# Kernel optimization log

Hardware: AMD Instinct MI355X
Metric: run time of the kernel (lower is better)

## Reference

```python
import jax, jax.numpy as jnp
import numpy as np

L = 4      # layer_num
H = 4      # n_head
C = 64     # emb_dim
E = 8      # ceil(512/65) Q/K channels per head
CV = 16    # emb_dim // n_head, V channels per head
FQ = 65    # n_freqs
EPS = 1e-5


def setup_inputs() -> dict:
    key = jax.random.key(0)
    ks = jax.random.split(key, 12)
    B, Tp, Tn = 4, 400, 400
    w = lambda k, shape, s=0.05: jax.random.normal(k, shape, jnp.float32) * s
    return {
        "pos_cond": jax.random.normal(ks[0], (B, C, Tp, FQ), jnp.float32),
        "neg_cond": jax.random.normal(ks[1], (B, C, Tn, FQ), jnp.float32),
        "seg_table": w(ks[2], (2, C * FQ), 0.02),
        # per-layer, per-head Q/K/V conv1x1 + PReLU + LayerNorm4DCF params
        "Qw": w(ks[3], (L, H, E, C)),  "Qb": jnp.zeros((L, H, E), jnp.float32),
        "Qa": jnp.full((L, H), 0.25, jnp.float32),
        "Qg": jnp.ones((L, H, E, FQ), jnp.float32), "Qbe": jnp.zeros((L, H, E, FQ), jnp.float32),
        "Kw": w(ks[4], (L, H, E, C)),  "Kb": jnp.zeros((L, H, E), jnp.float32),
        "Ka": jnp.full((L, H), 0.25, jnp.float32),
        "Kg": jnp.ones((L, H, E, FQ), jnp.float32), "Kbe": jnp.zeros((L, H, E, FQ), jnp.float32),
        "Vw": w(ks[5], (L, H, CV, C)), "Vb": jnp.zeros((L, H, CV), jnp.float32),
        "Va": jnp.full((L, H), 0.25, jnp.float32),
        "Vg": jnp.ones((L, H, CV, FQ), jnp.float32), "Vbe": jnp.zeros((L, H, CV, FQ), jnp.float32),
        # per-layer concat projection conv1x1 + PReLU + LayerNorm4DCF
        "Pw": w(ks[6], (L, C, C)), "Pb": jnp.zeros((L, C), jnp.float32),
        "Pa": jnp.full((L,), 0.25, jnp.float32),
        "Pg": jnp.ones((L, C, FQ), jnp.float32), "Pbe": jnp.zeros((L, C, FQ), jnp.float32),
    }


def _head_proj(x, W, b, a, g, be):
    # x: [B,C,T,F]; W: [H,O,C] -> y: [H,B,O,T,F]; conv1x1 + PReLU(scalar) + LN over (channel,freq)
    y = jnp.einsum('bctf,hoc->hbotf', x, W) + b[:, None, :, None, None]
    y = jnp.where(y >= 0, y, a[:, None, None, None, None] * y)
    mu = jnp.mean(y, axis=(2, 4), keepdims=True)
    var = jnp.var(y, axis=(2, 4), keepdims=True)
    return (y - mu) / jnp.sqrt(var + EPS) * g[:, None, :, None, :] + be[:, None, :, None, :]


def _attn_layer(x, Qw, Qb, Qa, Qg, Qbe, Kw, Kb, Ka, Kg, Kbe, Vw, Vb, Va, Vg, Vbe, Pw, Pb, Pa, Pg, Pbe):
    B, _, T, F = x.shape
    Q = _head_proj(x, Qw, Qb, Qa, Qg, Qbe)   # [H,B,E,T,F]
    K = _head_proj(x, Kw, Kb, Ka, Kg, Kbe)   # [H,B,E,T,F]
    V = _head_proj(x, Vw, Vb, Va, Vg, Vbe)   # [H,B,CV,T,F]
    Qf = jnp.transpose(Q, (0, 1, 3, 2, 4)).reshape(H, B, T, E * F)
    Kf = jnp.transpose(K, (0, 1, 3, 2, 4)).reshape(H, B, T, E * F)
    Vf = jnp.transpose(V, (0, 1, 3, 2, 4)).reshape(H, B, T, CV * F)
    d = Qf.shape[-1]
    attn = jax.nn.softmax(jnp.einsum('hbtd,hbsd->hbts', Qf, Kf) / jnp.sqrt(jnp.float32(d)), axis=-1)
    Of = jnp.einsum('hbts,hbsd->hbtd', attn, Vf)              # [H,B,T,CV*F]
    O = Of.reshape(H, B, T, CV, F)
    O = jnp.transpose(O, (1, 0, 3, 2, 4)).reshape(B, H * CV, T, F)  # concat heads on channel
    # concat projection: conv1x1 + PReLU + LN4DCF
    y = jnp.einsum('bctf,oc->botf', O, Pw) + Pb[None, :, None, None]
    y = jnp.where(y >= 0, y, Pa * y)
    mu = jnp.mean(y, axis=(1, 3), keepdims=True)
    var = jnp.var(y, axis=(1, 3), keepdims=True)
    return (y - mu) / jnp.sqrt(var + EPS) * Pg[None, :, None, :] + Pbe[None, :, None, :]


def reference(pos_cond, neg_cond, seg_table, Qw, Qb, Qa, Qg, Qbe, Kw, Kb, Ka, Kg, Kbe,
              Vw, Vb, Va, Vg, Vbe, Pw, Pb, Pa, Pg, Pbe):
    B, _, Tp, _ = pos_cond.shape
    Tn = neg_cond.shape[2]
    T = Tp + Tn
    x = jnp.concatenate([pos_cond, neg_cond], axis=2)          # [B,C,T,F]
    seg_idx = jnp.concatenate([jnp.zeros((Tp,), jnp.int32), jnp.ones((Tn,), jnp.int32)])
    seg = seg_table[seg_idx].reshape(T, C, FQ)                 # [T,C,F]
    x = x + jnp.transpose(seg, (1, 0, 2))[None]                # [1,C,T,F] broadcast over B
    fusion_shortcut = (0,)
    for li in range(L):
        y = _attn_layer(x, Qw[li], Qb[li], Qa[li], Qg[li], Qbe[li],
                        Kw[li], Kb[li], Ka[li], Kg[li], Kbe[li],
                        Vw[li], Vb[li], Va[li], Vg[li], Vbe[li],
                        Pw[li], Pb[li], Pa[li], Pg[li], Pbe[li])
        x = x + y if li in fusion_shortcut else y
    return x
```

## Files before the change

### kernel.cpp

```cpp
#include <hip/hip_runtime.h>

#define BB 4
#define CC 64
#define TT 800
#define FF 65
#define EE 8
#define CVV 16
#define HH 4

typedef __attribute__((ext_vector_type(8))) short short8;
typedef __attribute__((ext_vector_type(4))) float f32x4;

#define OT_SLAB (800 * 68 * 16)

__device__ __forceinline__ float bf2f(unsigned short u) {
  unsigned v = ((unsigned)u) << 16;
  return __builtin_bit_cast(float, v);
}
__device__ __forceinline__ unsigned short f2bf(float f) {
  unsigned u = __builtin_bit_cast(unsigned, f);
  unsigned r = (u + 0x7fffu + ((u >> 16) & 1u)) >> 16;
  return (unsigned short)r;
}

__device__ __forceinline__ void gll16(const void* g, void* l) {
  __builtin_amdgcn_global_load_lds(
      (const __attribute__((address_space(1))) void*)g,
      (__attribute__((address_space(3))) void*)l, 16, 0, 0);
}

__global__ __launch_bounds__(256) void buildx_kernel(
    const float* __restrict__ pos, const float* __restrict__ neg,
    const float* __restrict__ seg, float* __restrict__ X)
{
  size_t i = (size_t)blockIdx.x * 256 + threadIdx.x;
  const size_t total = (size_t)BB * CC * TT * FF;
  if (i >= total) return;
  int f = (int)(i % FF);
  size_t r = i / FF;
  int t = (int)(r % TT);
  size_t r2 = r / TT;
  int c = (int)(r2 % CC);
  int b = (int)(r2 / CC);
  float v; int si;
  if (t < 400) { v = pos[(((size_t)b * CC + c) * 400 + t) * FF + f]; si = 0; }
  else         { v = neg[(((size_t)b * CC + c) * 400 + (t - 400)) * FF + f]; si = 1; }
  X[i] = v + seg[(size_t)si * CC * FF + c * FF + f];
}

__global__ __launch_bounds__(256) void xt0_kernel(
    const float* __restrict__ X, unsigned short* __restrict__ Xt)
{
  __shared__ unsigned short tile[64][66];
  int b = blockIdx.y;
  int p0 = blockIdx.x * 64;
  int tid = threadIdx.x;
#pragma unroll
  for (int it = 0; it < 16; ++it) {
    int idx = it * 256 + tid;
    int c = idx >> 6, pp = idx & 63;
    int ps = p0 + pp;
    float v = (ps < 52000) ? X[((size_t)b * 64 + c) * 52000 + ps] : 0.f;
    tile[pp][c] = f2bf(v);
  }
  __syncthreads();
#pragma unroll
  for (int it = 0; it < 16; ++it) {
    int idx = it * 256 + tid;
    int pp = idx >> 6, c = idx & 63;
    int ps = p0 + pp;
    Xt[((size_t)b * 52032 + ps) * 64 + c] = tile[pp][c];
  }
}

__global__ __launch_bounds__(512) void qkv_gemm_kernel(
    const unsigned short* __restrict__ Xt,
    const float* __restrict__ Qw, const float* __restrict__ Qb, const float* __restrict__ Qa,
    const float* __restrict__ Qg, const float* __restrict__ Qbe,
    const float* __restrict__ Kw, const float* __restrict__ Kbi, const float* __restrict__ Ka,
    const float* __restrict__ Kg, const float* __restrict__ Kbe,
    const float* __restrict__ Vw, const float* __restrict__ Vb, const float* __restrict__ Va,
    const float* __restrict__ Vg, const float* __restrict__ Vbe,
    unsigned short* __restrict__ Qo, unsigned short* __restrict__ Ko,
    unsigned short* __restrict__ Vo, int li)
{
  __shared__ __align__(16) unsigned short lds[26624];
  unsigned short* lA = lds;

  int wg = (blockIdx.x & 7) * 100 + (blockIdx.x >> 3);
  int b = wg & 3, tb = wg >> 2;
  int tid = threadIdx.x;
  int lane = tid & 63, wid = tid >> 6;
  int tp = wid >> 2;
  int ws2 = wid & 3;
  int t0 = tb * 4 + tp * 2;
  unsigned short* lB = lds + 8192 + tp * 9216;

  for (int i = tid; i < 896; i += 512) {
    int u = i / 28, c = i - u * 28;
    int h = u >> 3, arr = (u >> 2) & 1, tt = u & 3;
    unsigned short* bp = arr ? Ko : Qo;
    unsigned* dst = (unsigned*)(bp + ((size_t)(h * 4 + b) * 896 + tb * 4 + tt) * 576) + 260 + c;
    *dst = 0u;
  }

  const float* Wq = Qw + (size_t)li * 2048;
  const float* Wk = Kw + (size_t)li * 2048;
  const float* Wv = Vw + (size_t)li * 4096;
#pragma unroll
  for (int q = 0; q < 2; ++q) {
    int chunk = q * 512 + tid;
    int row = chunk >> 3, c8 = chunk & 7;
    const float* src = (row < 32) ? (Wq + row * 64)
                     : (row < 64) ? (Wk + (row - 32) * 64)
                                  : (Wv + (row - 64) * 64);
    float4 f0 = *(const float4*)(src + c8 * 8);
    float4 f1 = *(const float4*)(src + c8 * 8 + 4);
    uint4 u;
    u.x = (unsigned)f2bf(f0.x) | ((unsigned)f2bf(f0.y) << 16);
    u.y = (unsigned)f2bf(f0.z) | ((unsigned)f2bf(f0.w) << 16);
    u.z = (unsigned)f2bf(f1.x) | ((unsigned)f2bf(f1.y) << 16);
    u.w = (unsigned)f2bf(f1.z) | ((unsigned)f2bf(f1.w) << 16);
    *(uint4*)&lA[row * 64 + ((c8 * 8) ^ ((row & 7) << 3))] = u;
  }
  const unsigned short* xb = Xt + ((size_t)b * 52032 + tb * 260) * 64;
#pragma unroll
  for (int q = 0; q < 5; ++q) {
    int chunk = q * 512 + tid;
    if (chunk < 2304) {
      int pair = (chunk >= 1152) ? 1 : 0;
      int ch = chunk - pair * 1152;
      int row = ch >> 3, c8 = ch & 7;
      uint4 u = *(const uint4*)&xb[(size_t)(pair * 130 + row) * 64 + c8 * 8];
      unsigned short* lbp = lds + 8192 + pair * 9216;
      *(uint4*)&lbp[row * 64 + ((c8 * 8) ^ ((row & 7) << 3))] = u;
    }
  }
  __syncthreads();

  f32x4 acc[2][9];
#pragma unroll
  for (int i = 0; i < 2; ++i)
#pragma unroll
    for (int j = 0; j < 9; ++j) acc[i][j] = {0.f, 0.f, 0.f, 0.f};
  const int fr = lane & 15, fk = lane >> 4;
  const int swz = (lane & 7) << 3;
#pragma unroll
  for (int kk = 0; kk < 2; ++kk) {
    int ko = (kk * 32 + fk * 8) ^ swz;
    short8 a0 = *(const short8*)&lA[(ws2 * 32 + fr) * 64 + ko];
    short8 a1 = *(const short8*)&lA[(ws2 * 32 + 16 + fr) * 64 + ko];
#pragma unroll
    for (int nf = 0; nf < 9; ++nf) {
      short8 bfr = *(const short8*)&lB[(nf * 16 + fr) * 64 + ko];
      acc[0][nf] = __builtin_amdgcn_mfma_f32_16x16x32_bf16(a0, bfr, acc[0][nf], 0, 0, 0);
      acc[1][nf] = __builtin_amdgcn_mfma_f32_16x16x32_bf16(a1, bfr, acc[1][nf], 0, 0, 0);
    }
  }
  __syncthreads();

  for (int it = 0; it < 17; ++it) {
    int i = it * 512 + tid;
    if (i < 8320) {
      int row = i / 65;
      float g, be;
      if (i < 2080)      { g = Qg[li * 2080 + i];          be = Qbe[li * 2080 + i]; }
      else if (i < 4160) { g = Kg[li * 2080 + (i - 2080)]; be = Kbe[li * 2080 + (i - 2080)]; }
      else               { g = Vg[li * 4160 + (i - 4160)]; be = Vbe[li * 4160 + (i - 4160)]; }
      unsigned pk = (unsigned)f2bf(g) | ((unsigned)f2bf(be) << 16);
      *(unsigned*)&lds[(i + row) * 2] = pk;
    }
  }

  int r4 = (lane >> 4) * 4;
  float mu0_[2], rs0_[2], mu1_[2], rs1_[2];
#pragma unroll
  for (int mf2 = 0; mf2 < 2; ++mf2) {
    int rbase = ws2 * 32 + mf2 * 16 + r4;
    float bias[4], alpha;
    if (rbase < 32) {
      alpha = Qa[li * 4 + (rbase >> 3)];
#pragma unroll
      for (int j = 0; j < 4; ++j) bias[j] = Qb[li * 32 + rbase + j];
    } else if (rbase < 64) {
      alpha = Ka[li * 4 + ((rbase - 32) >> 3)];
#pragma unroll
      for (int j = 0; j < 4; ++j) bias[j] = Kbi[li * 32 + rbase - 32 + j];
    } else {
      alpha = Va[li * 4 + ((rbase - 64) >> 4)];
#pragma unroll
      for (int j = 0; j < 4; ++j) bias[j] = Vb[li * 64 + rbase - 64 + j];
    }
    float s0 = 0.f, ss0 = 0.f, s1 = 0.f, ss1 = 0.f;
#pragma unroll
    for (int nf = 0; nf < 9; ++nf) {
      int col = nf * 16 + fr;
#pragma unroll
      for (int j = 0; j < 4; ++j) {
        float v = acc[mf2][nf][j] + bias[j];
        v = v >= 0.f ? v : alpha * v;
        acc[mf2][nf][j] = v;
        if (col < 65) { s0 += v; ss0 += v * v; }
        else if (col < 130) { s1 += v; ss1 += v * v; }
      }
    }
    if (ws2 < 2) {
#pragma unroll
      for (int off = 1; off < 32; off <<= 1) {
        s0 += __shfl_xor(s0, off); ss0 += __shfl_xor(ss0, off);
        s1 += __shfl_xor(s1, off); ss1 += __shfl_xor(ss1, off);
      }
    } else {
#pragma unroll
      for (int off = 1; off < 64; off <<= 1) {
        s0 += __shfl_xor(s0, off); ss0 += __shfl_xor(ss0, off);
        s1 += __shfl_xor(s1, off); ss1 += __shfl_xor(ss1, off);
      }
    }
    float invn = (ws2 < 2) ? (1.f / 520.f) : (1.f / 1040.f);
    float m0v = s0 * invn, m1v = s1 * invn;
    mu0_[mf2] = m0v; rs0_[mf2] = rsqrtf(ss0 * invn - m0v * m0v + 1e-5f);
    mu1_[mf2] = m1v; rs1_[mf2] = rsqrtf(ss1 * invn - m1v * m1v + 1e-5f);
  }
  __syncthreads();

#pragma unroll
  for (int mf2 = 0; mf2 < 2; ++mf2) {
#pragma unroll
    for (int j = 0; j < 4; ++j) {
      int row = ws2 * 32 + mf2 * 16 + r4 + j;
      unsigned short* dst; int LD;
      if (row < 32) {
        dst = Qo + ((size_t)((row >> 3) * 4 + b) * 896 + t0) * 576 + (row & 7) * 65; LD = 576;
      } else if (row < 64) {
        int rk = row - 32;
        dst = Ko + ((size_t)((rk >> 3) * 4 + b) * 896 + t0) * 576 + (rk & 7) * 65; LD = 576;
      } else {
        int rv = row - 64;
        dst = Vo + ((size_t)((rv >> 4) * 4 + b) * 800 + t0) * 1040 + (rv & 15) * 65; LD = 1040;
      }
      int grow = row * 132;
#pragma unroll
      for (int nf = 0; nf < 9; ++nf) {
        int col = nf * 16 + fr;
        if (col >= 130) continue;
        int half = (col >= 65) ? 1 : 0;
        int f = col - half * 65;
        unsigned pk = *(const unsigned*)&lds[grow + f * 2];
        float g = bf2f((unsigned short)(pk & 0xffff));
        float be = bf2f((unsigned short)(pk >> 16));
        float mu = half ? mu1_[mf2] : mu0_[mf2];
        float rs = half ? rs1_[mf2] : rs0_[mf2];
        dst[(size_t)half * LD + f] = f2bf((acc[mf2][nf][j] - mu) * rs * g + be);
      }
    }
  }
}

__global__ __launch_bounds__(256) void vtrans_kernel(
    const unsigned short* __restrict__ V, unsigned short* __restrict__ Vt)
{
  __shared__ unsigned short tile[64][66];
  int z = blockIdx.z;
  const unsigned short* Vp = V + (size_t)z * 800 * 1040;
  unsigned short* Vtp = Vt + (size_t)z * 1152 * 832;
  int t0 = blockIdx.x * 64, n0 = blockIdx.y * 64;
  int tid = threadIdx.x;
#pragma unroll
  for (int it = 0; it < 16; ++it) {
    int idx = it * 256 + tid;
    int r = idx >> 6, c = idx & 63;
    int t = t0 + r, n = n0 + c;
    tile[r][c] = (t < 800 && n < 1040) ? Vp[(size_t)t * 1040 + n] : (unsigned short)0;
  }
  __syncthreads();
#pragma unroll
  for (int it = 0; it < 16; ++it) {
    int idx = it * 256 + tid;
    int r = idx >> 6, c = idx & 63;
    int n = n0 + r;
    if (n < 1040) {
      int cv = n / 65, f5 = n - cv * 65;
      Vtp[(size_t)(f5 * 16 + cv) * 832 + t0 + c] = tile[c][r];
    }
  }
}

template <int LDA, int LDB, int KSTEPS>
__device__ __forceinline__ void gemm128(
    const unsigned short* __restrict__ Ag, const unsigned short* __restrict__ Bg,
    int m0, int n0, unsigned short* lA, unsigned short* lB, f32x4 acc[4][4])
{
  const int tid = threadIdx.x;
  const int lane = tid & 63;
  const int wid = tid >> 6;
  const int wm = wid >> 1, wn = wid & 1;

  const int fr = lane & 15, fk = lane >> 4;
  const int swz = (lane & 7) << 3;
  const int srow = lane >> 3;
  const int gc8 = (lane & 7) ^ srow;
  int aoff[4][2], boff[4][2];
#pragma unroll
  for (int mf = 0; mf < 4; ++mf)
#pragma unroll
    for (int kk = 0; kk < 2; ++kk) {
      aoff[mf][kk] = (wm * 64 + mf * 16 + fr) * 64 + ((kk * 32 + fk * 8) ^ swz);
      boff[mf][kk] = (wn * 64 + mf * 16 + fr) * 64 + ((kk * 32 + fk * 8) ^ swz);
    }

  const unsigned short* gA = Ag + (size_t)m0 * LDA;
  const unsigned short* gB = Bg + (size_t)n0 * LDB;

  for (int ks = 0; ks < KSTEPS; ++ks) {
    int k0 = ks * 64;
    __syncthreads();
#pragma unroll
    for (int i = 0; i < 4; ++i) {
      int r0 = wid * 32 + i * 8;
      gll16(&gA[(size_t)(r0 + srow) * LDA + k0 + gc8 * 8], &lA[r0 * 64]);
      gll16(&gB[(size_t)(r0 + srow) * LDB + k0 + gc8 * 8], &lB[r0 * 64]);
    }
    __syncthreads();
#pragma unroll
    for (int kk = 0; kk < 2; ++kk) {
      short8 a[4], b[4];
#pragma unroll
      for (int i = 0; i < 4; ++i) {
        a[i] = *(const short8*)&lA[aoff[i][kk]];
        b[i] = *(const short8*)&lB[boff[i][kk]];
      }
#pragma unroll
      for (int i = 0; i < 4; ++i)
#pragma unroll
        for (int j = 0; j < 4; ++j)
          acc[i][j] = __builtin_amdgcn_mfma_f32_16x16x32_bf16(a[i], b[j], acc[i][j], 0, 0, 0);
    }
  }
}

__global__ __launch_bounds__(256) void qk_mfma_kernel(
    const unsigned short* __restrict__ Q, const unsigned short* __restrict__ K,
    unsigned short* __restrict__ SP)
{
  __shared__ __align__(16) unsigned short lA[128 * 64];
  __shared__ __align__(16) unsigned short lB[128 * 64];
  int wg = (blockIdx.x & 7) * 98 + (blockIdx.x >> 3);
  int z = wg / 49, r = wg % 49;
  int nt = r / 7, mt = r % 7;
  const unsigned short* Ag = Q + (size_t)z * 896 * 576;
  const unsigned short* Bg = K + (size_t)z * 896 * 576;
  int m0 = mt * 128, n0 = nt * 128;
  f32x4 acc[4][4];
#pragma unroll
  for (int i = 0; i < 4; ++i)
#pragma unroll
    for (int j = 0; j < 4; ++j) acc[i][j] = {0.f, 0.f, 0.f, 0.f};
  gemm128<576, 576, 9>(Ag, Bg, m0, n0, lA, lB, acc);
  const int lane = threadIdx.x & 63, wid = threadIdx.x >> 6;
  const int wm = wid >> 1, wn = wid & 1;
  unsigned short* Sp = SP + (size_t)z * 896 * 832;
  const float scale = 0.04385290096535146f;
#pragma unroll
  for (int mf = 0; mf < 4; ++mf)
#pragma unroll
    for (int nf = 0; nf < 4; ++nf) {
      int n = n0 + wn * 64 + nf * 16 + (lane & 15);
      if (n >= 800) continue;
#pragma unroll
      for (int j = 0; j < 4; ++j) {
        int m = m0 + wm * 64 + mf * 16 + (lane >> 4) * 4 + j;
        if (m < 800) Sp[(size_t)m * 832 + n] = f2bf(acc[mf][nf][j] * scale);
      }
    }
}

__global__ __launch_bounds__(256) void softmax_bf16_kernel(unsigned short* __restrict__ SP)
{
  int wid = threadIdx.x >> 6, lane = threadIdx.x & 63;
  int row = blockIdx.x * 4 + wid;
  int z = row / 800, r = row - z * 800;
  unsigned short* p = SP + (size_t)z * 896 * 832 + (size_t)r * 832;
  float v[13];
  float mx = -1e30f;
#pragma unroll
  for (int i = 0; i < 13; ++i) {
    int col = i * 64 + lane;
    float x = (col < 800) ? bf2f(p[col]) : -1e30f;
    v[i] = x;
    mx = fmaxf(mx, x);
  }
#pragma unroll
  for (int off = 32; off; off >>= 1) mx = fmaxf(mx, __shfl_xor(mx, off));
  float s = 0.f;
#pragma unroll
  for (int i = 0; i < 13; ++i) { v[i] = __expf(v[i] - mx); s += v[i]; }
#pragma unroll
  for (int off = 32; off; off >>= 1) s += __shfl_xor(s, off);
  float inv = 1.0f / s;
#pragma unroll
  for (int i = 0; i < 13; ++i) {
    int col = i * 64 + lane;
    if (col < 832) p[col] = f2bf(v[i] * inv);
  }
}

__global__ __launch_bounds__(256) void pv_mfma_kernel(
    const unsigned short* __restrict__ SP, const unsigned short* __restrict__ Vt,
    unsigned short* __restrict__ Ot)
{
  __shared__ __align__(16) unsigned short lA[128 * 64];
  __shared__ __align__(16) unsigned short lB[128 * 64];
  int wg = (blockIdx.x & 7) * 126 + (blockIdx.x >> 3);
  int z = wg / 63, r = wg % 63;
  int nt = r / 7, mt = r % 7;
  const unsigned short* Ag = SP + (size_t)z * 896 * 832;
  const unsigned short* Bg = Vt + (size_t)z * 1152 * 832;
  int m0 = mt * 128, n0 = nt * 128;
  f32x4 acc[4][4];
#pragma unroll
  for (int i = 0; i < 4; ++i)
#pragma unroll
    for (int j = 0; j < 4; ++j) acc[i][j] = {0.f, 0.f, 0.f, 0.f};
  gemm128<832, 832, 13>(Ag, Bg, m0, n0, lA, lB, acc);
  const int lane = threadIdx.x & 63, wid = threadIdx.x >> 6;
  const int wm = wid >> 1, wn = wid & 1;
  int h = z >> 2, bb = z & 3;
  unsigned short* Op = Ot + (size_t)(bb * 4 + h) * OT_SLAB;
#pragma unroll
  for (int mf = 0; mf < 4; ++mf)
#pragma unroll
    for (int nf = 0; nf < 4; ++nf) {
      int n = n0 + wn * 64 + nf * 16 + (lane & 15);
      if (n >= 1040) continue;
      int f5 = n >> 4, cv = n & 15;
#pragma unroll
      for (int j = 0; j < 4; ++j) {
        int m = m0 + wm * 64 + mf * 16 + (lane >> 4) * 4 + j;
        if (m < 800) Op[((size_t)m * 68 + f5) * 16 + cv] = f2bf(acc[mf][nf][j]);
      }
    }
}

__global__ __launch_bounds__(512) void pproj_gemm_kernel(
    const unsigned short* __restrict__ Ot,
    const float* __restrict__ Pw, const float* __restrict__ Pb,
    const float* __restrict__ Pa, const float* __restrict__ Pg, const float* __restrict__ Pbe,
    const float* __restrict__ X, float* __restrict__ out,
    unsigned short* __restrict__ Xt, int li)
{
  __shared__ __align__(16) float smem[16768];
  __shared__ float redbuf[8][4];
  unsigned short* sA = (unsigned short*)smem;

  int wg = (blockIdx.x & 7) * 100 + (blockIdx.x >> 3);
  int b = wg & 3, tb = wg >> 2;
  int tid = threadIdx.x, lane = tid & 63, wid = tid >> 6;
  int tp = wid >> 2;
  int ws = wid & 3;
  unsigned short* sB = sA + 4096 + tp * 9216;

  const float* pw = Pw + (size_t)li * 4096;
  {
    int row = tid >> 3, c8 = tid & 7;
    float4 f0 = *(const float4*)(pw + row * 64 + c8 * 8);
    float4 f1 = *(const float4*)(pw + row * 64 + c8 * 8 + 4);
    uint4 u;
    u.x = (unsigned)f2bf(f0.x) | ((unsigned)f2bf(f0.y) << 16);
    u.y = (unsigned)f2bf(f0.z) | ((unsigned)f2bf(f0.w) << 16);
    u.z = (unsigned)f2bf(f1.x) | ((unsigned)f2bf(f1.y) << 16);
    u.w = (unsigned)f2bf(f1.z) | ((unsigned)f2bf(f1.w) << 16);
    *(uint4*)&sA[row * 64 + ((c8 * 8) ^ ((row & 7) << 3))] = u;
  }
  const unsigned short* ob = Ot + (size_t)b * 4 * OT_SLAB;
#pragma unroll
  for (int q = 0; q < 5; ++q) {
    int chunk = q * 512 + tid;
    if (chunk < 2304) {
      int pair = (chunk >= 1152) ? 1 : 0;
      int ch = chunk - pair * 1152;
      int row = ch >> 3, c8 = ch & 7;
      int half = (row >= 65) ? 1 : 0;
      int f = row - half * 65;
      int tt = tb * 4 + pair * 2 + half;
      uint4 u = *(const uint4*)&ob[(size_t)(c8 >> 1) * OT_SLAB +
                                   ((size_t)tt * 68 + f) * 16 + (c8 & 1) * 8];
      unsigned short* sbp = sA + 4096 + pair * 9216;
      *(uint4*)&sbp[row * 64 + ((c8 * 8) ^ ((row & 7) << 3))] = u;
    }
  }
  __syncthreads();

  f32x4 acc[9];
#pragma unroll
  for (int j = 0; j < 9; ++j) acc[j] = {0.f, 0.f, 0.f, 0.f};
  const int fr = lane & 15, fk = lane >> 4;
  const int swz = (lane & 7) << 3;
#pragma unroll
  for (int kk = 0; kk < 2; ++kk) {
    int ko = (kk * 32 + fk * 8) ^ swz;
    short8 a = *(const short8*)&sA[(ws * 16 + fr) * 64 + ko];
#pragma unroll
    for (int nf = 0; nf < 9; ++nf) {
      short8 bb2 = *(const short8*)&sB[(nf * 16 + fr) * 64 + ko];
      acc[nf] = __builtin_amdgcn_mfma_f32_16x16x32_bf16(a, bb2, acc[nf], 0, 0, 0);
    }
  }

  float alpha = Pa[li];
  int rbase = ws * 16 + (lane >> 4) * 4;
  float bias[4];
#pragma unroll
  for (int j = 0; j < 4; ++j) bias[j] = Pb[li * 64 + rbase + j];
  float s0 = 0.f, ss0 = 0.f, s1 = 0.f, ss1 = 0.f;
#pragma unroll
  for (int nf = 0; nf < 9; ++nf) {
    int col = nf * 16 + fr;
#pragma unroll
    for (int j = 0; j < 4; ++j) {
      float v = acc[nf][j] + bias[j];
      v = v >= 0.f ? v : alpha * v;
      acc[nf][j] = v;
      if (col < 65) { s0 += v; ss0 += v * v; }
      else if (col < 130) { s1 += v; ss1 += v * v; }
    }
  }
#pragma unroll
  for (int off = 32; off; off >>= 1) {
    s0 += __shfl_xor(s0, off); ss0 += __shfl_xor(ss0, off);
    s1 += __shfl_xor(s1, off); ss1 += __shfl_xor(ss1, off);
  }
  if (lane == 0) {
    redbuf[wid][0] = s0; redbuf[wid][1] = ss0;
    redbuf[wid][2] = s1; redbuf[wid][3] = ss1;
  }
  __syncthreads();
  int rb0 = tp * 4;
  float S0 = redbuf[rb0][0] + redbuf[rb0+1][0] + redbuf[rb0+2][0] + redbuf[rb0+3][0];
  float SS0 = redbuf[rb0][1] + redbuf[rb0+1][1] + redbuf[rb0+2][1] + redbuf[rb0+3][1];
  float S1 = redbuf[rb0][2] + redbuf[rb0+1][2] + redbuf[rb0+2][2] + redbuf[rb0+3][2];
  float SS1 = redbuf[rb0][3] + redbuf[rb0+1][3] + redbuf[rb0+2][3] + redbuf[rb0+3][3];
  const float invn = 1.f / 4160.f;
  float mu0 = S0 * invn, rs0 = rsqrtf(SS0 * invn - mu0 * mu0 + 1e-5f);
  float mu1 = S1 * invn, rs1 = rsqrtf(SS1 * invn - mu1 * mu1 + 1e-5f);

  float* Yfp = smem + tp * 8384;
  const float* pg  = Pg  + (size_t)li * 4160;
  const float* pbe = Pbe + (size_t)li * 4160;
  int posp = tb * 260 + tp * 130;
#pragma unroll
  for (int nf = 0; nf < 9; ++nf) {
    int col = nf * 16 + fr;
    if (col >= 130) continue;
    int half = (col >= 65) ? 1 : 0;
    int f5 = col - half * 65;
    float mu = half ? mu1 : mu0, rs = half ? rs1 : rs0;
#pragma unroll
    for (int j = 0; j < 4; ++j) {
      int oc = rbase + j;
      float v = (acc[nf][j] - mu) * rs * pg[oc * 65 + f5] + pbe[oc * 65 + f5];
      if (li == 0) v += X[(size_t)(b * 64 + oc) * 52000 + posp + col];
      Yfp[oc * 131 + col] = v;
    }
  }
  __syncthreads();

  if (li < 3) {
    int oc = tid & 63, pq = tid >> 6;
#pragma unroll
    for (int it = 0; it < 33; ++it) {
      int p2 = it * 8 + pq;
      if (p2 < 260) {
        int pair = (p2 >= 130) ? 1 : 0;
        int pp = p2 - pair * 130;
        Xt[((size_t)b * 52032 + tb * 260 + p2) * 64 + oc] =
            f2bf(smem[pair * 8384 + oc * 131 + pp]);
      }
    }
  } else {
    int pair = (tid >= 130) ? 1 : 0;
    int pp = tid - pair * 130;
    for (int oc = 0; oc < 64; ++oc) {
      if (tid < 260)
        out[(size_t)(b * 64 + oc) * 52000 + tb * 260 + tid] =
            smem[pair * 8384 + oc * 131 + pp];
    }
  }
}

extern "C" void kernel_launch(void* const* d_in, const int* in_sizes, int n_in,
                              void* d_out, int out_size, void* d_ws, size_t ws_size,
                              hipStream_t stream) {
  const float* pos = (const float*)d_in[0];
  const float* neg = (const float*)d_in[1];
  const float* seg = (const float*)d_in[2];
  const float* Qw  = (const float*)d_in[3];
  const float* Qb  = (const float*)d_in[4];
  const float* Qa  = (const float*)d_in[5];
  const float* Qg  = (const float*)d_in[6];
  const float* Qbe = (const float*)d_in[7];
  const float* Kw  = (const float*)d_in[8];
  const float* Kbi = (const float*)d_in[9];
  const float* Ka  = (const float*)d_in[10];
  const float* Kg  = (const float*)d_in[11];
  const float* Kbe = (const float*)d_in[12];
  const float* Vw  = (const float*)d_in[13];
  const float* Vb  = (const float*)d_in[14];
  const float* Va  = (const float*)d_in[15];
  const float* Vg  = (const float*)d_in[16];
  const float* Vbe = (const float*)d_in[17];
  const float* Pw  = (const float*)d_in[18];
  const float* Pb  = (const float*)d_in[19];
  const float* Pa  = (const float*)d_in[20];
  const float* Pg  = (const float*)d_in[21];
  const float* Pbe = (const float*)d_in[22];
  float* out = (float*)d_out;
  char* base = (char*)d_ws;

  float* X = (float*)base;
  unsigned short* Xt16 = (unsigned short*)(base + 53248000);
  unsigned short* SP16 = (unsigned short*)(base + 79888384);
  unsigned short* Vt16 = (unsigned short*)(base + 103743488);
  unsigned short* V16  = (unsigned short*)(base + 134414336);
  unsigned short* Qb16 = (unsigned short*)(base + 161038336);
  unsigned short* Kb16 = (unsigned short*)(base + 177553408);
  unsigned short* Ot16 = (unsigned short*)(base + 161038336);

  dim3 blk(256);
  const size_t XN = (size_t)BB * CC * TT * FF;
  buildx_kernel<<<(unsigned)((XN + 255) / 256), blk, 0, stream>>>(pos, neg, seg, X);
  xt0_kernel<<<dim3(813, 4), blk, 0, stream>>>(X, Xt16);
  for (int li = 0; li < 4; ++li) {
    qkv_gemm_kernel<<<800, dim3(512), 0, stream>>>(Xt16, Qw, Qb, Qa, Qg, Qbe,
                                                   Kw, Kbi, Ka, Kg, Kbe,
                                                   Vw, Vb, Va, Vg, Vbe,
                                                   Qb16, Kb16, V16, li);
    vtrans_kernel<<<dim3(13, 17, 16), blk, 0, stream>>>(V16, Vt16);
    qk_mfma_kernel<<<784, blk, 0, stream>>>(Qb16, Kb16, SP16);
    softmax_bf16_kernel<<<3200, blk, 0, stream>>>(SP16);
    pv_mfma_kernel<<<1008, blk, 0, stream>>>(SP16, Vt16, Ot16);
    pproj_gemm_kernel<<<800, dim3(512), 0, stream>>>(Ot16, Pw, Pb, Pa, Pg, Pbe,
                                                     X, out, Xt16, li);
  }
}
```

Baseline: 720.2 us.

## Use direct global-to-LDS loads and write bf16 projection output straight from registers

```diff
diff --git a/kernel.cpp b/kernel.cpp
--- a/kernel.cpp
+++ b/kernel.cpp
@@ -102,6 +102,21 @@
     unsigned short* bp = arr ? Ko : Qo;
     unsigned* dst = (unsigned*)(bp + ((size_t)(h * 4 + b) * 896 + tb * 4 + tt) * 576) + 260 + c;
     *dst = 0u;
+  }
+
+  const unsigned short* xb = Xt + ((size_t)b * 52032 + tb * 260) * 64;
+  const int srow = lane >> 3;
+  const int gc8s = (lane & 7) ^ srow;
+#pragma unroll
+  for (int it = 0; it < 5; ++it) {
+    int s = it * 8 + wid;
+    if (s < 36) {
+      int pair = (s >= 18) ? 1 : 0;
+      int r0 = (s - pair * 18) * 8;
+      int row = r0 + srow;
+      gll16(&xb[(size_t)(pair * 130 + row) * 64 + gc8s * 8],
+            lds + 8192 + pair * 9216 + r0 * 64);
+    }
   }
 
   const float* Wq = Qw + (size_t)li * 2048;
@@ -123,19 +138,6 @@
     u.w = (unsigned)f2bf(f1.z) | ((unsigned)f2bf(f1.w) << 16);
     *(uint4*)&lA[row * 64 + ((c8 * 8) ^ ((row & 7) << 3))] = u;
   }
-  const unsigned short* xb = Xt + ((size_t)b * 52032 + tb * 260) * 64;
-#pragma unroll
-  for (int q = 0; q < 5; ++q) {
-    int chunk = q * 512 + tid;
-    if (chunk < 2304) {
-      int pair = (chunk >= 1152) ? 1 : 0;
-      int ch = chunk - pair * 1152;
-      int row = ch >> 3, c8 = ch & 7;
-      uint4 u = *(const uint4*)&xb[(size_t)(pair * 130 + row) * 64 + c8 * 8];
-      unsigned short* lbp = lds + 8192 + pair * 9216;
-      *(uint4*)&lbp[row * 64 + ((c8 * 8) ^ ((row & 7) << 3))] = u;
-    }
-  }
   __syncthreads();
 
   f32x4 acc[2][9];
@@ -449,9 +451,11 @@
     const float* __restrict__ X, float* __restrict__ out,
     unsigned short* __restrict__ Xt, int li)
 {
-  __shared__ __align__(16) float smem[16768];
+  __shared__ __align__(16) unsigned short lds[30848];
   __shared__ float redbuf[8][4];
-  unsigned short* sA = (unsigned short*)smem;
+  unsigned short* sA = lds;
+  unsigned* gb = (unsigned*)(lds + 22528);
+  float* Yf = (float*)lds;
 
   int wg = (blockIdx.x & 7) * 100 + (blockIdx.x >> 3);
   int b = wg & 3, tb = wg >> 2;
@@ -460,6 +464,26 @@
   int ws = wid & 3;
   unsigned short* sB = sA + 4096 + tp * 9216;
 
+  const unsigned short* ob = Ot + (size_t)b * 4 * OT_SLAB;
+  const int srow = lane >> 3;
+  const int gc8 = (lane & 7) ^ srow;
+  {
+    int hh = gc8 >> 1, cvh = gc8 & 1;
+#pragma unroll
+    for (int it = 0; it < 5; ++it) {
+      int s = it * 8 + wid;
+      if (s < 36) {
+        int pair = (s >= 18) ? 1 : 0;
+        int r0 = (s - pair * 18) * 8;
+        int row = r0 + srow;
+        int half = (row >= 65) ? 1 : 0;
+        int f = row - half * 65;
+        int tt = tb * 4 + pair * 2 + half;
+        gll16(&ob[(size_t)hh * OT_SLAB + ((size_t)tt * 68 + f) * 16 + cvh * 8],
+              sA + 4096 + pair * 9216 + r0 * 64);
+      }
+    }
+  }
   const float* pw = Pw + (size_t)li * 4096;
   {
     int row = tid >> 3, c8 = tid & 7;
@@ -472,23 +496,6 @@
     u.w = (unsigned)f2bf(f1.z) | ((unsigned)f2bf(f1.w) << 16);
     *(uint4*)&sA[row * 64 + ((c8 * 8) ^ ((row & 7) << 3))] = u;
   }
-  const unsigned short* ob = Ot + (size_t)b * 4 * OT_SLAB;
-#pragma unroll
-  for (int q = 0; q < 5; ++q) {
-    int chunk = q * 512 + tid;
-    if (chunk < 2304) {
-      int pair = (chunk >= 1152) ? 1 : 0;
-      int ch = chunk - pair * 1152;
-      int row = ch >> 3, c8 = ch & 7;
-      int half = (row >= 65) ? 1 : 0;
-      int f = row - half * 65;
-      int tt = tb * 4 + pair * 2 + half;
-      uint4 u = *(const uint4*)&ob[(size_t)(c8 >> 1) * OT_SLAB +
-                                   ((size_t)tt * 68 + f) * 16 + (c8 & 1) * 8];
-      unsigned short* sbp = sA + 4096 + pair * 9216;
-      *(uint4*)&sbp[row * 64 + ((c8 * 8) ^ ((row & 7) << 3))] = u;
-    }
-  }
   __syncthreads();
 
   f32x4 acc[9];
@@ -505,6 +512,12 @@
       short8 bb2 = *(const short8*)&sB[(nf * 16 + fr) * 64 + ko];
       acc[nf] = __builtin_amdgcn_mfma_f32_16x16x32_bf16(a, bb2, acc[nf], 0, 0, 0);
     }
+  }
+
+  for (int it = 0; it < 9; ++it) {
+    int i = it * 512 + tid;
+    if (i < 4160)
+      gb[i] = (unsigned)f2bf(Pg[li * 4160 + i]) | ((unsigned)f2bf(Pbe[li * 4160 + i]) << 16);
   }
 
   float alpha = Pa[li];
@@ -544,46 +557,58 @@
   float mu0 = S0 * invn, rs0 = rsqrtf(SS0 * invn - mu0 * mu0 + 1e-5f);
   float mu1 = S1 * invn, rs1 = rsqrtf(SS1 * invn - mu1 * mu1 + 1e-5f);
 
-  float* Yfp = smem + tp * 8384;
-  const float* pg  = Pg  + (size_t)li * 4160;
-  const float* pbe = Pbe + (size_t)li * 4160;
-  int posp = tb * 260 + tp * 130;
-#pragma unroll
-  for (int nf = 0; nf < 9; ++nf) {
-    int col = nf * 16 + fr;
-    if (col >= 130) continue;
-    int half = (col >= 65) ? 1 : 0;
-    int f5 = col - half * 65;
-    float mu = half ? mu1 : mu0, rs = half ? rs1 : rs0;
-#pragma unroll
-    for (int j = 0; j < 4; ++j) {
-      int oc = rbase + j;
-      float v = (acc[nf][j] - mu) * rs * pg[oc * 65 + f5] + pbe[oc * 65 + f5];
-      if (li == 0) v += X[(size_t)(b * 64 + oc) * 52000 + posp + col];
-      Yfp[oc * 131 + col] = v;
-    }
-  }
-  __syncthreads();
-
+  int posrow = tb * 260 + tp * 130;
   if (li < 3) {
-    int oc = tid & 63, pq = tid >> 6;
-#pragma unroll
-    for (int it = 0; it < 33; ++it) {
-      int p2 = it * 8 + pq;
-      if (p2 < 260) {
-        int pair = (p2 >= 130) ? 1 : 0;
-        int pp = p2 - pair * 130;
-        Xt[((size_t)b * 52032 + tb * 260 + p2) * 64 + oc] =
-            f2bf(smem[pair * 8384 + oc * 131 + pp]);
-      }
+#pragma unroll
+    for (int nf = 0; nf < 9; ++nf) {
+      int col = nf * 16 + fr;
+      if (col >= 130) continue;
+      int half = (col >= 65) ? 1 : 0;
+      int f5 = col - half * 65;
+      float mu = half ? mu1 : mu0, rs = half ? rs1 : rs0;
+      float vv[4];
+#pragma unroll
+      for (int j = 0; j < 4; ++j) {
+        int oc = rbase + j;
+        unsigned pk = gb[oc * 65 + f5];
+        float g = bf2f((unsigned short)(pk & 0xffff));
+        float be = bf2f((unsigned short)(pk >> 16));
+        float v = (acc[nf][j] - mu) * rs * g + be;
+        if (li == 0) v += X[(size_t)(b * 64 + oc) * 52000 + posrow + col];
+        vv[j] = v;
+      }
+      uint2 u;
+      u.x = (unsigned)f2bf(vv[0]) | ((unsigned)f2bf(vv[1]) << 16);
+      u.y = (unsigned)f2bf(vv[2]) | ((unsigned)f2bf(vv[3]) << 16);
+      *(uint2*)&Xt[((size_t)b * 52032 + posrow + col) * 64 + rbase] = u;
     }
   } else {
-    int pair = (tid >= 130) ? 1 : 0;
-    int pp = tid - pair * 130;
-    for (int oc = 0; oc < 64; ++oc) {
-      if (tid < 260)
-        out[(size_t)(b * 64 + oc) * 52000 + tb * 260 + tid] =
-            smem[pair * 8384 + oc * 131 + pp];
+    for (int pair = 0; pair < 2; ++pair) {
+      __syncthreads();
+      if (tp == pair) {
+#pragma unroll
+        for (int nf = 0; nf < 9; ++nf) {
+          int col = nf * 16 + fr;
+          if (col >= 130) continue;
+          int half = (col >= 65) ? 1 : 0;
+          int f5 = col - half * 65;
+          float mu = half ? mu1 : mu0, rs = half ? rs1 : rs0;
+#pragma unroll
+          for (int j = 0; j < 4; ++j) {
+            int oc = rbase + j;
+            unsigned pk = gb[oc * 65 + f5];
+            float g = bf2f((unsigned short)(pk & 0xffff));
+            float be = bf2f((unsigned short)(pk >> 16));
+            Yf[oc * 131 + col] = (acc[nf][j] - mu) * rs * g + be;
+          }
+        }
+      }
+      __syncthreads();
+      if (tid < 130) {
+        for (int oc = 0; oc < 64; ++oc)
+          out[(size_t)(b * 64 + oc) * 52000 + tb * 260 + pair * 130 + tid] =
+              Yf[oc * 131 + tid];
+      }
     }
   }
 }
```

New measurement: 718.4 us. About the same (-0.2%).

## Fuse output projection with next layer's QKV projection and async-load X tiles

Applied to the files above, without the earlier changes.

```diff
diff --git a/kernel.cpp b/kernel.cpp
--- a/kernel.cpp
+++ b/kernel.cpp
@@ -11,7 +11,7 @@
 typedef __attribute__((ext_vector_type(8))) short short8;
 typedef __attribute__((ext_vector_type(4))) float f32x4;
 
-#define OT_SLAB (800 * 68 * 16)
+#define OT_SLAB (800 * 65 * 16)
 
 __device__ __forceinline__ float bf2f(unsigned short u) {
   unsigned v = ((unsigned)u) << 16;
@@ -104,6 +104,21 @@
     *dst = 0u;
   }
 
+  const unsigned short* xb = Xt + ((size_t)b * 52032 + tb * 260) * 64;
+  const int srow = lane >> 3;
+  const int gc8s = (lane & 7) ^ srow;
+#pragma unroll
+  for (int it = 0; it < 5; ++it) {
+    int s = it * 8 + wid;
+    if (s < 36) {
+      int pair = (s >= 18) ? 1 : 0;
+      int r0 = (s - pair * 18) * 8;
+      int row = r0 + srow;
+      gll16(&xb[(size_t)(pair * 130 + row) * 64 + gc8s * 8],
+            lds + 8192 + pair * 9216 + r0 * 64);
+    }
+  }
+
   const float* Wq = Qw + (size_t)li * 2048;
   const float* Wk = Kw + (size_t)li * 2048;
   const float* Wv = Vw + (size_t)li * 4096;
@@ -123,19 +138,6 @@
     u.w = (unsigned)f2bf(f1.z) | ((unsigned)f2bf(f1.w) << 16);
     *(uint4*)&lA[row * 64 + ((c8 * 8) ^ ((row & 7) << 3))] = u;
   }
-  const unsigned short* xb = Xt + ((size_t)b * 52032 + tb * 260) * 64;
-#pragma unroll
-  for (int q = 0; q < 5; ++q) {
-    int chunk = q * 512 + tid;
-    if (chunk < 2304) {
-      int pair = (chunk >= 1152) ? 1 : 0;
-      int ch = chunk - pair * 1152;
-      int row = ch >> 3, c8 = ch & 7;
-      uint4 u = *(const uint4*)&xb[(size_t)(pair * 130 + row) * 64 + c8 * 8];
-      unsigned short* lbp = lds + 8192 + pair * 9216;
-      *(uint4*)&lbp[row * 64 + ((c8 * 8) ^ ((row & 7) << 3))] = u;
-    }
-  }
   __syncthreads();
 
   f32x4 acc[2][9];
@@ -437,21 +439,30 @@
 #pragma unroll
       for (int j = 0; j < 4; ++j) {
         int m = m0 + wm * 64 + mf * 16 + (lane >> 4) * 4 + j;
-        if (m < 800) Op[((size_t)m * 68 + f5) * 16 + cv] = f2bf(acc[mf][nf][j]);
-      }
-    }
-}
-
-__global__ __launch_bounds__(512) void pproj_gemm_kernel(
+        if (m < 800) Op[((size_t)m * 65 + f5) * 16 + cv] = f2bf(acc[mf][nf][j]);
+      }
+    }
+}
+
+__global__ __launch_bounds__(512) void fused_pproj_qkv_kernel(
     const unsigned short* __restrict__ Ot,
     const float* __restrict__ Pw, const float* __restrict__ Pb,
     const float* __restrict__ Pa, const float* __restrict__ Pg, const float* __restrict__ Pbe,
-    const float* __restrict__ X, float* __restrict__ out,
-    unsigned short* __restrict__ Xt, int li)
+    const float* __restrict__ X,
+    const float* __restrict__ Qw, const float* __restrict__ Qb, const float* __restrict__ Qa,
+    const float* __restrict__ Qg, const float* __restrict__ Qbe,
+    const float* __restrict__ Kw, const float* __restrict__ Kbi, const float* __restrict__ Ka,
+    const float* __restrict__ Kg, const float* __restrict__ Kbe,
+    const float* __restrict__ Vw, const float* __restrict__ Vb, const float* __restrict__ Va,
+    const float* __restrict__ Vg, const float* __restrict__ Vbe,
+    unsigned short* __restrict__ Qo, unsigned short* __restrict__ Ko,
+    unsigned short* __restrict__ Vo, int li)
 {
-  __shared__ __align__(16) float smem[16768];
+  __shared__ __align__(16) unsigned short lds[30720];
   __shared__ float redbuf[8][4];
-  unsigned short* sA = (unsigned short*)smem;
+  unsigned short* sA = lds;
+  unsigned short* lA2 = lds + 22528;
+  const int lq = li + 1;
 
   int wg = (blockIdx.x & 7) * 100 + (blockIdx.x >> 3);
   int b = wg & 3, tb = wg >> 2;
@@ -460,6 +471,31 @@
   int ws = wid & 3;
   unsigned short* sB = sA + 4096 + tp * 9216;
 
+  for (int i = tid; i < 896; i += 512) {
+    int u = i / 28, c = i - u * 28;
+    int h = u >> 3, arr = (u >> 2) & 1, tt = u & 3;
+    unsigned short* bp = arr ? Ko : Qo;
+    unsigned* dst = (unsigned*)(bp + ((size_t)(h * 4 + b) * 896 + tb * 4 + tt) * 576) + 260 + c;
+    *dst = 0u;
+  }
+
+  const unsigned short* ob = Ot + (size_t)b * 4 * OT_SLAB;
+#pragma unroll
+  for (int q = 0; q < 5; ++q) {
+    int chunk = q * 512 + tid;
+    if (chunk < 2304) {
+      int pair = (chunk >= 1152) ? 1 : 0;
+      int ch = chunk - pair * 1152;
+      int row = ch >> 3, c8 = ch & 7;
+      int half = (row >= 65) ? 1 : 0;
+      int f = row - half * 65;
+      int tt = tb * 4 + pair * 2 + half;
+      uint4 u = *(const uint4*)&ob[(size_t)(c8 >> 1) * OT_SLAB +
+                                   ((size_t)tt * 65 + f) * 16 + (c8 & 1) * 8];
+      unsigned short* sbp = sA + 4096 + pair * 9216;
+      *(uint4*)&sbp[row * 64 + ((c8 * 8) ^ ((row & 7) << 3))] = u;
+    }
+  }
   const float* pw = Pw + (size_t)li * 4096;
   {
     int row = tid >> 3, c8 = tid & 7;
@@ -472,6 +508,254 @@
     u.w = (unsigned)f2bf(f1.z) | ((unsigned)f2bf(f1.w) << 16);
     *(uint4*)&sA[row * 64 + ((c8 * 8) ^ ((row & 7) << 3))] = u;
   }
+  const float* Wq = Qw + (size_t)lq * 2048;
+  const float* Wk = Kw + (size_t)lq * 2048;
+  const float* Wv = Vw + (size_t)lq * 4096;
+#pragma unroll
+  for (int q = 0; q < 2; ++q) {
+    int chunk = q * 512 + tid;
+    int row = chunk >> 3, c8 = chunk & 7;
+    const float* src = (row < 32) ? (Wq + row * 64)
+                     : (row < 64) ? (Wk + (row - 32) * 64)
+                                  : (Wv + (row - 64) * 64);
+    float4 f0 = *(const float4*)(src + c8 * 8);
+    float4 f1 = *(const float4*)(src + c8 * 8 + 4);
+    uint4 u;
+    u.x = (unsigned)f2bf(f0.x) | ((unsigned)f2bf(f0.y) << 16);
+    u.y = (unsigned)f2bf(f0.z) | ((unsigned)f2bf(f0.w) << 16);
+    u.z = (unsigned)f2bf(f1.x) | ((unsigned)f2bf(f1.y) << 16);
+    u.w = (unsigned)f2bf(f1.z) | ((unsigned)f2bf(f1.w) << 16);
+    *(uint4*)&lA2[row * 64 + ((c8 * 8) ^ ((row & 7) << 3))] = u;
+  }
+  __syncthreads();
+
+  f32x4 acc[9];
+#pragma unroll
+  for (int j = 0; j < 9; ++j) acc[j] = {0.f, 0.f, 0.f, 0.f};
+  const int fr = lane & 15, fk = lane >> 4;
+  const int swz = (lane & 7) << 3;
+#pragma unroll
+  for (int kk = 0; kk < 2; ++kk) {
+    int ko = (kk * 32 + fk * 8) ^ swz;
+    short8 a = *(const short8*)&sA[(ws * 16 + fr) * 64 + ko];
+#pragma unroll
+    for (int nf = 0; nf < 9; ++nf) {
+      short8 bb2 = *(const short8*)&sB[(nf * 16 + fr) * 64 + ko];
+      acc[nf] = __builtin_amdgcn_mfma_f32_16x16x32_bf16(a, bb2, acc[nf], 0, 0, 0);
+    }
+  }
+
+  float alpha = Pa[li];
+  int rbase = ws * 16 + (lane >> 4) * 4;
+  float bias[4];
+#pragma unroll
+  for (int j = 0; j < 4; ++j) bias[j] = Pb[li * 64 + rbase + j];
+  float s0 = 0.f, ss0 = 0.f, s1 = 0.f, ss1 = 0.f;
+#pragma unroll
+  for (int nf = 0; nf < 9; ++nf) {
+    int col = nf * 16 + fr;
+#pragma unroll
+    for (int j = 0; j < 4; ++j) {
+      float v = acc[nf][j] + bias[j];
+      v = v >= 0.f ? v : alpha * v;
+      acc[nf][j] = v;
+      if (col < 65) { s0 += v; ss0 += v * v; }
+      else if (col < 130) { s1 += v; ss1 += v * v; }
+    }
+  }
+#pragma unroll
+  for (int off = 32; off; off >>= 1) {
+    s0 += __shfl_xor(s0, off); ss0 += __shfl_xor(ss0, off);
+    s1 += __shfl_xor(s1, off); ss1 += __shfl_xor(ss1, off);
+  }
+  if (lane == 0) {
+    redbuf[wid][0] = s0; redbuf[wid][1] = ss0;
+    redbuf[wid][2] = s1; redbuf[wid][3] = ss1;
+  }
+  __syncthreads();
+  int rb0 = tp * 4;
+  float S0 = redbuf[rb0][0] + redbuf[rb0+1][0] + redbuf[rb0+2][0] + redbuf[rb0+3][0];
+  float SS0 = redbuf[rb0][1] + redbuf[rb0+1][1] + redbuf[rb0+2][1] + redbuf[rb0+3][1];
+  float S1 = redbuf[rb0][2] + redbuf[rb0+1][2] + redbuf[rb0+2][2] + redbuf[rb0+3][2];
+  float SS1 = redbuf[rb0][3] + redbuf[rb0+1][3] + redbuf[rb0+2][3] + redbuf[rb0+3][3];
+  const float invn = 1.f / 4160.f;
+  float mu0 = S0 * invn, rs0 = rsqrtf(SS0 * invn - mu0 * mu0 + 1e-5f);
+  float mu1 = S1 * invn, rs1 = rsqrtf(SS1 * invn - mu1 * mu1 + 1e-5f);
+
+  int posrow = tb * 260 + tp * 130;
+  unsigned short* ypan = sB;
+  const float* pg  = Pg  + (size_t)li * 4160;
+  const float* pbe = Pbe + (size_t)li * 4160;
+#pragma unroll
+  for (int nf = 0; nf < 9; ++nf) {
+    int col = nf * 16 + fr;
+    if (col >= 130) continue;
+    int half = (col >= 65) ? 1 : 0;
+    int f5 = col - half * 65;
+    float mu = half ? mu1 : mu0, rs = half ? rs1 : rs0;
+    float vv[4];
+#pragma unroll
+    for (int j = 0; j < 4; ++j) {
+      int oc = rbase + j;
+      float v = (acc[nf][j] - mu) * rs * pg[oc * 65 + f5] + pbe[oc * 65 + f5];
+      if (li == 0) v += X[(size_t)(b * 64 + oc) * 52000 + posrow + col];
+      vv[j] = v;
+    }
+    uint2 u;
+    u.x = (unsigned)f2bf(vv[0]) | ((unsigned)f2bf(vv[1]) << 16);
+    u.y = (unsigned)f2bf(vv[2]) | ((unsigned)f2bf(vv[3]) << 16);
+    int idx = col * 64 + (((rbase & ~7)) ^ ((col & 7) << 3)) + (rbase & 7);
+    *(uint2*)&ypan[idx] = u;
+  }
+  __syncthreads();
+
+  f32x4 acc2[2][9];
+#pragma unroll
+  for (int i = 0; i < 2; ++i)
+#pragma unroll
+    for (int j = 0; j < 9; ++j) acc2[i][j] = {0.f, 0.f, 0.f, 0.f};
+#pragma unroll
+  for (int kk = 0; kk < 2; ++kk) {
+    int ko = (kk * 32 + fk * 8) ^ swz;
+    short8 a0 = *(const short8*)&lA2[(ws * 32 + fr) * 64 + ko];
+    short8 a1 = *(const short8*)&lA2[(ws * 32 + 16 + fr) * 64 + ko];
+#pragma unroll
+    for (int nf = 0; nf < 9; ++nf) {
+      short8 bfr = *(const short8*)&ypan[(nf * 16 + fr) * 64 + ko];
+      acc2[0][nf] = __builtin_amdgcn_mfma_f32_16x16x32_bf16(a0, bfr, acc2[0][nf], 0, 0, 0);
+      acc2[1][nf] = __builtin_amdgcn_mfma_f32_16x16x32_bf16(a1, bfr, acc2[1][nf], 0, 0, 0);
+    }
+  }
+  __syncthreads();
+
+  for (int it = 0; it < 17; ++it) {
+    int i = it * 512 + tid;
+    if (i < 8320) {
+      int row = i / 65;
+      float g, be;
+      if (i < 2080)      { g = Qg[lq * 2080 + i];          be = Qbe[lq * 2080 + i]; }
+      else if (i < 4160) { g = Kg[lq * 2080 + (i - 2080)]; be = Kbe[lq * 2080 + (i - 2080)]; }
+      else               { g = Vg[lq * 4160 + (i - 4160)]; be = Vbe[lq * 4160 + (i - 4160)]; }
+      unsigned pk = (unsigned)f2bf(g) | ((unsigned)f2bf(be) << 16);
+      *(unsigned*)&lds[(i + row) * 2] = pk;
+    }
+  }
+
+  int r4 = (lane >> 4) * 4;
+  int t0 = tb * 4 + tp * 2;
+  float mu0_[2], rs0_[2], mu1_[2], rs1_[2];
+#pragma unroll
+  for (int mf2 = 0; mf2 < 2; ++mf2) {
+    int rb = ws * 32 + mf2 * 16 + r4;
+    float bias2[4], alpha2;
+    if (rb < 32) {
+      alpha2 = Qa[lq * 4 + (rb >> 3)];
+#pragma unroll
+      for (int j = 0; j < 4; ++j) bias2[j] = Qb[lq * 32 + rb + j];
+    } else if (rb < 64) {
+      alpha2 = Ka[lq * 4 + ((rb - 32) >> 3)];
+#pragma unroll
+      for (int j = 0; j < 4; ++j) bias2[j] = Kbi[lq * 32 + rb - 32 + j];
+    } else {
+      alpha2 = Va[lq * 4 + ((rb - 64) >> 4)];
+#pragma unroll
+      for (int j = 0; j < 4; ++j) bias2[j] = Vb[lq * 64 + rb - 64 + j];
+    }
+    float t_s0 = 0.f, t_ss0 = 0.f, t_s1 = 0.f, t_ss1 = 0.f;
+#pragma unroll
+    for (int nf = 0; nf < 9; ++nf) {
+      int col = nf * 16 + fr;
+#pragma unroll
+      for (int j = 0; j < 4; ++j) {
+        float v = acc2[mf2][nf][j] + bias2[j];
+        v = v >= 0.f ? v : alpha2 * v;
+        acc2[mf2][nf][j] = v;
+        if (col < 65) { t_s0 += v; t_ss0 += v * v; }
+        else if (col < 130) { t_s1 += v; t_ss1 += v * v; }
+      }
+    }
+    if (ws < 2) {
+#pragma unroll
+      for (int off = 1; off < 32; off <<= 1) {
+        t_s0 += __shfl_xor(t_s0, off); t_ss0 += __shfl_xor(t_ss0, off);
+        t_s1 += __shfl_xor(t_s1, off); t_ss1 += __shfl_xor(t_ss1, off);
+      }
+    } else {
+#pragma unroll
+      for (int off = 1; off < 64; off <<= 1) {
+        t_s0 += __shfl_xor(t_s0, off); t_ss0 += __shfl_xor(t_ss0, off);
+        t_s1 += __shfl_xor(t_s1, off); t_ss1 += __shfl_xor(t_ss1, off);
+      }
+    }
+    float invn2 = (ws < 2) ? (1.f / 520.f) : (1.f / 1040.f);
+    float m0v = t_s0 * invn2, m1v = t_s1 * invn2;
+    mu0_[mf2] = m0v; rs0_[mf2] = rsqrtf(t_ss0 * invn2 - m0v * m0v + 1e-5f);
+    mu1_[mf2] = m1v; rs1_[mf2] = rsqrtf(t_ss1 * invn2 - m1v * m1v + 1e-5f);
+  }
+  __syncthreads();
+
+#pragma unroll
+  for (int mf2 = 0; mf2 < 2; ++mf2) {
+#pragma unroll
+    for (int j = 0; j < 4; ++j) {
+      int row = ws * 32 + mf2 * 16 + r4 + j;
+      unsigned short* dst; int LD;
+      if (row < 32) {
+        dst = Qo + ((size_t)((row >> 3) * 4 + b) * 896 + t0) * 576 + (row & 7) * 65; LD = 576;
+      } else if (row < 64) {
+        int rk = row - 32;
+        dst = Ko + ((size_t)((rk >> 3) * 4 + b) * 896 + t0) * 576 + (rk & 7) * 65; LD = 576;
+      } else {
+        int rv = row - 64;
+        dst = Vo + ((size_t)((rv >> 4) * 4 + b) * 800 + t0) * 1040 + (rv & 15) * 65; LD = 1040;
+      }
+      int grow = row * 132;
+#pragma unroll
+      for (int nf = 0; nf < 9; ++nf) {
+        int col = nf * 16 + fr;
+        if (col >= 130) continue;
+        int half = (col >= 65) ? 1 : 0;
+        int f = col - half * 65;
+        unsigned pk = *(const unsigned*)&lds[grow + f * 2];
+        float g = bf2f((unsigned short)(pk & 0xffff));
+        float be = bf2f((unsigned short)(pk >> 16));
+        float mu = half ? mu1_[mf2] : mu0_[mf2];
+        float rs = half ? rs1_[mf2] : rs0_[mf2];
+        dst[(size_t)half * LD + f] = f2bf((acc2[mf2][nf][j] - mu) * rs * g + be);
+      }
+    }
+  }
+}
+
+__global__ __launch_bounds__(512) void pproj3_kernel(
+    const unsigned short* __restrict__ Ot,
+    const float* __restrict__ Pw, const float* __restrict__ Pb,
+    const float* __restrict__ Pa, const float* __restrict__ Pg, const float* __restrict__ Pbe,
+    float* __restrict__ out, int li)
+{
+  __shared__ __align__(16) float smem[16768];
+  __shared__ float redbuf[8][4];
+  unsigned short* sA = (unsigned short*)smem;
+
+  int wg = (blockIdx.x & 7) * 100 + (blockIdx.x >> 3);
+  int b = wg & 3, tb = wg >> 2;
+  int tid = threadIdx.x, lane = tid & 63, wid = tid >> 6;
+  int tp = wid >> 2;
+  int ws = wid & 3;
+  unsigned short* sB = sA + 4096 + tp * 9216;
+
+  const float* pw = Pw + (size_t)li * 4096;
+  {
+    int row = tid >> 3, c8 = tid & 7;
+    float4 f0 = *(const float4*)(pw + row * 64 + c8 * 8);
+    float4 f1 = *(const float4*)(pw + row * 64 + c8 * 8 + 4);
+    uint4 u;
+    u.x = (unsigned)f2bf(f0.x) | ((unsigned)f2bf(f0.y) << 16);
+    u.y = (unsigned)f2bf(f0.z) | ((unsigned)f2bf(f0.w) << 16);
+    u.z = (unsigned)f2bf(f1.x) | ((unsigned)f2bf(f1.y) << 16);
+    u.w = (unsigned)f2bf(f1.z) | ((unsigned)f2bf(f1.w) << 16);
+    *(uint4*)&sA[row * 64 + ((c8 * 8) ^ ((row & 7) << 3))] = u;
+  }
   const unsigned short* ob = Ot + (size_t)b * 4 * OT_SLAB;
 #pragma unroll
   for (int q = 0; q < 5; ++q) {
@@ -484,7 +768,7 @@
       int f = row - half * 65;
       int tt = tb * 4 + pair * 2 + half;
       uint4 u = *(const uint4*)&ob[(size_t)(c8 >> 1) * OT_SLAB +
-                                   ((size_t)tt * 68 + f) * 16 + (c8 & 1) * 8];
+                                   ((size_t)tt * 65 + f) * 16 + (c8 & 1) * 8];
       unsigned short* sbp = sA + 4096 + pair * 9216;
       *(uint4*)&sbp[row * 64 + ((c8 * 8) ^ ((row & 7) << 3))] = u;
     }
@@ -547,7 +831,6 @@
   float* Yfp = smem + tp * 8384;
   const float* pg  = Pg  + (size_t)li * 4160;
   const float* pbe = Pbe + (size_t)li * 4160;
-  int posp = tb * 260 + tp * 130;
 #pragma unroll
   for (int nf = 0; nf < 9; ++nf) {
     int col = nf * 16 + fr;
@@ -558,33 +841,17 @@
 #pragma unroll
     for (int j = 0; j < 4; ++j) {
       int oc = rbase + j;
-      float v = (acc[nf][j] - mu) * rs * pg[oc * 65 + f5] + pbe[oc * 65 + f5];
-      if (li == 0) v += X[(size_t)(b * 64 + oc) * 52000 + posp + col];
-      Yfp[oc * 131 + col] = v;
-    }
-  }
-  __syncthreads();
-
-  if (li < 3) {
-    int oc = tid & 63, pq = tid >> 6;
-#pragma unroll
-    for (int it = 0; it < 33; ++it) {
-      int p2 = it * 8 + pq;
-      if (p2 < 260) {
-        int pair = (p2 >= 130) ? 1 : 0;
-        int pp = p2 - pair * 130;
-        Xt[((size_t)b * 52032 + tb * 260 + p2) * 64 + oc] =
-            f2bf(smem[pair * 8384 + oc * 131 + pp]);
-      }
-    }
-  } else {
-    int pair = (tid >= 130) ? 1 : 0;
-    int pp = tid - pair * 130;
-    for (int oc = 0; oc < 64; ++oc) {
-      if (tid < 260)
-        out[(size_t)(b * 64 + oc) * 52000 + tb * 260 + tid] =
-            smem[pair * 8384 + oc * 131 + pp];
-    }
+      Yfp[oc * 131 + col] = (acc[nf][j] - mu) * rs * pg[oc * 65 + f5] + pbe[oc * 65 + f5];
+    }
+  }
+  __syncthreads();
+
+  int pair = (tid >= 130) ? 1 : 0;
+  int pp = tid - pair * 130;
+  for (int oc = 0; oc < 64; ++oc) {
+    if (tid < 260)
+      out[(size_t)(b * 64 + oc) * 52000 + tb * 260 + tid] =
+          smem[pair * 8384 + oc * 131 + pp];
   }
 }
 
@@ -619,27 +886,33 @@
 
   float* X = (float*)base;
   unsigned short* Xt16 = (unsigned short*)(base + 53248000);
+  unsigned short* Ot16 = (unsigned short*)(base + 53248000);
   unsigned short* SP16 = (unsigned short*)(base + 79888384);
   unsigned short* Vt16 = (unsigned short*)(base + 103743488);
   unsigned short* V16  = (unsigned short*)(base + 134414336);
   unsigned short* Qb16 = (unsigned short*)(base + 161038336);
   unsigned short* Kb16 = (unsigned short*)(base + 177553408);
-  unsigned short* Ot16 = (unsigned short*)(base + 161038336);
 
   dim3 blk(256);
   const size_t XN = (size_t)BB * CC * TT * FF;
   buildx_kernel<<<(unsigned)((XN + 255) / 256), blk, 0, stream>>>(pos, neg, seg, X);
   xt0_kernel<<<dim3(813, 4), blk, 0, stream>>>(X, Xt16);
+  qkv_gemm_kernel<<<800, dim3(512), 0, stream>>>(Xt16, Qw, Qb, Qa, Qg, Qbe,
+                                                 Kw, Kbi, Ka, Kg, Kbe,
+                                                 Vw, Vb, Va, Vg, Vbe,
+                                                 Qb16, Kb16, V16, 0);
   for (int li = 0; li < 4; ++li) {
-    qkv_gemm_kernel<<<800, dim3(512), 0, stream>>>(Xt16, Qw, Qb, Qa, Qg, Qbe,
-                                                   Kw, Kbi, Ka, Kg, Kbe,
-                                                   Vw, Vb, Va, Vg, Vbe,
-                                                   Qb16, Kb16, V16, li);
     vtrans_kernel<<<dim3(13, 17, 16), blk, 0, stream>>>(V16, Vt16);
     qk_mfma_kernel<<<784, blk, 0, stream>>>(Qb16, Kb16, SP16);
     softmax_bf16_kernel<<<3200, blk, 0, stream>>>(SP16);
     pv_mfma_kernel<<<1008, blk, 0, stream>>>(SP16, Vt16, Ot16);
-    pproj_gemm_kernel<<<800, dim3(512), 0, stream>>>(Ot16, Pw, Pb, Pa, Pg, Pbe,
-                                                     X, out, Xt16, li);
-  }
-}
+    if (li < 3) {
+      fused_pproj_qkv_kernel<<<800, dim3(512), 0, stream>>>(
+          Ot16, Pw, Pb, Pa, Pg, Pbe, X,
+          Qw, Qb, Qa, Qg, Qbe, Kw, Kbi, Ka, Kg, Kbe, Vw, Vb, Va, Vg, Vbe,
+          Qb16, Kb16, V16, li);
+    } else {
+      pproj3_kernel<<<800, dim3(512), 0, stream>>>(Ot16, Pw, Pb, Pa, Pg, Pbe, out, 3);
+    }
+  }
+}
```

Result: slower. 776.8 us (+7.9%).
